# Kernel tuning notes

Measured on AMD Instinct MI355X. Metric: run time of the kernel, lower is better.

The kernel has to match this reference:

```python
import jax, jax.numpy as jnp
import numpy as np

EPS = 1e-6
BASE_THETA = 10000.0


def setup_inputs() -> dict:
    key = jax.random.key(0)
    ks = jax.random.split(key, 6)
    S, E = 4096, 4096
    scale = 1.0 / np.sqrt(E)
    return {
        "x": jax.random.normal(ks[0], (S, E), dtype=jnp.float32),
        "w_q": jax.random.normal(ks[1], (E, E), dtype=jnp.float32) * scale,
        "w_k": jax.random.normal(ks[2], (E, E), dtype=jnp.float32) * scale,
        "w_v": jax.random.normal(ks[3], (E, E), dtype=jnp.float32) * scale,
        "w_out": jax.random.normal(ks[4], (E, E), dtype=jnp.float32) * scale,
        "scaling_factor": jax.random.uniform(ks[5], (E,), dtype=jnp.float32, minval=0.5, maxval=1.5),
    }


def _rope_apply(t, cos, sin):
    # t: (S, D) fp16; cos/sin: (S, D//2) fp16. Closed form of the per-position
    # block-diagonal 2x2 rotation matrix matmul in the original loop:
    # out[2j]   =  t[2j]*cos + t[2j+1]*sin
    # out[2j+1] = -t[2j]*sin + t[2j+1]*cos
    S, D = t.shape
    t2 = t.reshape(S, D // 2, 2)
    even, odd = t2[..., 0], t2[..., 1]
    out = jnp.stack([even * cos + odd * sin, -even * sin + odd * cos], axis=-1)
    return out.reshape(S, D)


def reference(x, w_q, w_k, w_v, w_out, scaling_factor):
    f16, f32 = jnp.float16, jnp.float32
    S, E = x.shape
    # __init__: q / q_inv / head rotations are identity; quantize = cast fp16 (scale 1).
    # q_inv * scaling_factor.view(1,-1) == diag(scaling_factor) -> row-scale weights.
    wq = (scaling_factor[:, None] * w_q).astype(f16)
    wk = (scaling_factor[:, None] * w_k).astype(f16)
    wv = (scaling_factor[:, None] * w_v).astype(f16)
    wo = w_out.astype(f16)

    # input @ identity; rms_norm in fp32
    xn = x * jax.lax.rsqrt(jnp.mean(x * x, axis=-1, keepdims=True) + EPS)
    xq = xn.astype(f16)

    # quantized matmuls: fp16 operands, fp32 accumulation, cast back to fp16
    q = (xq.astype(f32) @ wq.astype(f32)).astype(f16)
    k = (xq.astype(f32) @ wk.astype(f32)).astype(f16)
    v = (xq.astype(f32) @ wv.astype(f32)).astype(f16)

    # RoPE over full feature dim (size = E), vectorized over positions
    pos = jnp.arange(S, dtype=f32)[:, None]
    j = jnp.arange(E // 2, dtype=f32)[None, :]
    theta = pos / jnp.power(BASE_THETA, 2.0 * j / E)
    cos = jnp.cos(theta).astype(f16)
    sin = jnp.sin(theta).astype(f16)
    q = _rope_apply(q, cos, sin)
    k = _rope_apply(k, cos, sin)

    # rot_head_k_tiled is identity -> quantize is just fp16 cast (already fp16)
    scores = (q.astype(f32) @ k.T.astype(f32)).astype(f16)
    scores = scores / np.float16(np.sqrt(E))
    # causal mask: strict upper triangle -> -inf
    row = jnp.arange(S)[:, None]
    col = jnp.arange(S)[None, :]
    scores = jnp.where(col > row, jnp.float16(-jnp.inf), scores)
    attn_w = jax.nn.softmax(scores, axis=1)
    attn = attn_w @ v  # fp16 matmul as in original

    out = (attn.astype(f32) @ wo.astype(f32)).astype(f16)
    return out
```

## Files before the change

kernel.cpp:

```cpp
#include <hip/hip_runtime.h>
#include <hip/hip_bf16.h>
#include <cmath>


typedef _Float16 f16;
typedef _Float16 f16x4 __attribute__((ext_vector_type(4)));
typedef _Float16 f16x8 __attribute__((ext_vector_type(8)));
typedef float f32x4 __attribute__((ext_vector_type(4)));

#define S_DIM 4096
#define E_DIM 4096

__device__ __forceinline__ void gload_lds16(const void* g, void* l) {
  __builtin_amdgcn_global_load_lds((const __attribute__((address_space(1))) void*)g,
                                   (__attribute__((address_space(3))) void*)l,
                                   16, 0, 0);
}

__global__ __launch_bounds__(256) void rmsnorm_f16(const float* __restrict__ x,
                                                   f16* __restrict__ xq, int E) {
  const int row = blockIdx.x;
  const int t = threadIdx.x;
  const float4* xr = (const float4*)(x + (size_t)row * E);
  float4 v[4];
  float ss = 0.f;
#pragma unroll
  for (int i = 0; i < 4; ++i) {
    v[i] = xr[t + 256 * i];
    ss += v[i].x * v[i].x + v[i].y * v[i].y + v[i].z * v[i].z + v[i].w * v[i].w;
  }
#pragma unroll
  for (int o = 1; o < 64; o <<= 1) ss += __shfl_xor(ss, o);
  __shared__ float red[4];
  const int wid = t >> 6, lane = t & 63;
  if (lane == 0) red[wid] = ss;
  __syncthreads();
  const float tot = red[0] + red[1] + red[2] + red[3];
  const float r = 1.0f / sqrtf(tot / (float)E + 1e-6f);
  f16* xo = xq + (size_t)row * E;
#pragma unroll
  for (int i = 0; i < 4; ++i) {
    f16x4 o;
    o[0] = (f16)(v[i].x * r);
    o[1] = (f16)(v[i].y * r);
    o[2] = (f16)(v[i].z * r);
    o[3] = (f16)(v[i].w * r);
    *(f16x4*)(xo + 4 * (t + 256 * i)) = o;
  }
}

__global__ __launch_bounds__(256) void wconv_t(const float* __restrict__ W,
                                               const float* __restrict__ s,
                                               f16* __restrict__ WT, int N) {
  __shared__ f16 tile[64][65];
  const int tr = blockIdx.y * 64;
  const int tc = blockIdx.x * 64;
  const int t = threadIdx.x;
  const int r = t / 16;
  const int c4 = (t % 16) * 4;
#pragma unroll
  for (int i = 0; i < 4; ++i) {
    const int row = r + i * 16;
    float4 w = *(const float4*)(W + (size_t)(tr + row) * N + tc + c4);
    const float sc = s ? s[tr + row] : 1.0f;
    tile[row][c4 + 0] = (f16)(w.x * sc);
    tile[row][c4 + 1] = (f16)(w.y * sc);
    tile[row][c4 + 2] = (f16)(w.z * sc);
    tile[row][c4 + 3] = (f16)(w.w * sc);
  }
  __syncthreads();
#pragma unroll
  for (int i = 0; i < 4; ++i) {
    const int row = r + i * 16;
    f16x4 o;
    o[0] = tile[c4 + 0][row];
    o[1] = tile[c4 + 1][row];
    o[2] = tile[c4 + 2][row];
    o[3] = tile[c4 + 3][row];
    *(f16x4*)(WT + (size_t)(tc + row) * N + tr + c4) = o;
  }
}

__global__ __launch_bounds__(256) void transpose_f16(const f16* __restrict__ V,
                                                     f16* __restrict__ VT,
                                                     int R, int C) {
  __shared__ f16 tile[64][65];
  const int tr = blockIdx.y * 64;
  const int tc = blockIdx.x * 64;
  const int t = threadIdx.x;
  const int r = t / 16;
  const int c4 = (t % 16) * 4;
#pragma unroll
  for (int i = 0; i < 4; ++i) {
    const int row = r + i * 16;
    f16x4 in = *(const f16x4*)(V + (size_t)(tr + row) * C + tc + c4);
    tile[row][c4 + 0] = in[0];
    tile[row][c4 + 1] = in[1];
    tile[row][c4 + 2] = in[2];
    tile[row][c4 + 3] = in[3];
  }
  __syncthreads();
#pragma unroll
  for (int i = 0; i < 4; ++i) {
    const int row = r + i * 16;
    f16x4 o;
    o[0] = tile[c4 + 0][row];
    o[1] = tile[c4 + 1][row];
    o[2] = tile[c4 + 2][row];
    o[3] = tile[c4 + 3][row];
    *(f16x4*)(VT + (size_t)(tc + row) * R + tr + c4) = o;
  }
}

__global__ __launch_bounds__(256) void freq_tab_k(float* __restrict__ tab) {
  const int j = blockIdx.x * 256 + threadIdx.x;
  if (j < 2048) tab[j] = (float)pow(10000.0, (double)j / 2048.0);
}

__global__ __launch_bounds__(256) void rope_qk(f16* __restrict__ q,
                                               f16* __restrict__ k,
                                               const float* __restrict__ ftab,
                                               int E) {
  const int idx = blockIdx.x * 256 + threadIdx.x;
  const int cpr = E / 8;
  const int pos = idx / cpr;
  const int ch = idx % cpr;
  const int j0 = ch * 4;
  const float fpos = (float)pos;
  f16x8 qv = *(f16x8*)(q + (size_t)idx * 8);
  f16x8 kv = *(f16x8*)(k + (size_t)idx * 8);
  f16x8 qo, ko;
#pragma unroll
  for (int p = 0; p < 4; ++p) {
    const int j = j0 + p;
    const float th = fpos / ftab[j];
    float sn, cs;
    sincosf(th, &sn, &cs);
    const f16 c16 = (f16)cs, s16 = (f16)sn;
    const float c = (float)c16, s = (float)s16;
    {
      const float e = (float)qv[2 * p], o = (float)qv[2 * p + 1];
      const f16 t1 = (f16)(e * c), t2 = (f16)(o * s);
      const f16 u1 = (f16)(-(e * s)), u2 = (f16)(o * c);
      qo[2 * p] = (f16)((float)t1 + (float)t2);
      qo[2 * p + 1] = (f16)((float)u1 + (float)u2);
    }
    {
      const float e = (float)kv[2 * p], o = (float)kv[2 * p + 1];
      const f16 t1 = (f16)(e * c), t2 = (f16)(o * s);
      const f16 u1 = (f16)(-(e * s)), u2 = (f16)(o * c);
      ko[2 * p] = (f16)((float)t1 + (float)t2);
      ko[2 * p + 1] = (f16)((float)u1 + (float)u2);
    }
  }
  *(f16x8*)(q + (size_t)idx * 8) = qo;
  *(f16x8*)(k + (size_t)idx * 8) = ko;
}

__global__ __launch_bounds__(256) void softmax_causal(f16* __restrict__ sc, int S) {
  const int row = blockIdx.x;
  const int t = threadIdx.x;
  f16* p = sc + (size_t)row * S;
  float v[16];
  bool msk[16];
#pragma unroll
  for (int i = 0; i < 2; ++i) {
    f16x8 a = *(const f16x8*)(p + (size_t)(i * 256 + t) * 8);
#pragma unroll
    for (int j = 0; j < 8; ++j) v[i * 8 + j] = (float)a[j];
  }
  float m = -1e30f;
#pragma unroll
  for (int i = 0; i < 2; ++i)
#pragma unroll
    for (int j = 0; j < 8; ++j) {
      const int col = (i * 256 + t) * 8 + j;
      const int ii = i * 8 + j;
      msk[ii] = (col > row);
      if (!msk[ii]) m = fmaxf(m, v[ii]);
    }
#pragma unroll
  for (int o = 1; o < 64; o <<= 1) m = fmaxf(m, __shfl_xor(m, o));
  __shared__ float red[4];
  const int wid = t >> 6, lane = t & 63;
  if (lane == 0) red[wid] = m;
  __syncthreads();
  m = fmaxf(fmaxf(red[0], red[1]), fmaxf(red[2], red[3]));
  __syncthreads();
  f16 e16[16];
  float sum = 0.f;
#pragma unroll
  for (int i = 0; i < 16; ++i) {
    if (msk[i]) {
      e16[i] = (f16)0.0f;
    } else {
      const f16 d16 = (f16)(v[i] - m);
      e16[i] = (f16)expf((float)d16);
      sum += (float)e16[i];
    }
  }
#pragma unroll
  for (int o = 1; o < 64; o <<= 1) sum += __shfl_xor(sum, o);
  if (lane == 0) red[wid] = sum;
  __syncthreads();
  sum = red[0] + red[1] + red[2] + red[3];
  const f16 den16 = (f16)sum;
  const float den = (float)den16;
#pragma unroll
  for (int i = 0; i < 2; ++i) {
    f16x8 o;
#pragma unroll
    for (int j = 0; j < 8; ++j) {
      const int ii = i * 8 + j;
      o[j] = msk[ii] ? (f16)0.0f : (f16)((float)e16[ii] / den);
    }
    *(f16x8*)(p + (size_t)(i * 256 + t) * 8) = o;
  }
}

__device__ __forceinline__ void store_out(f16* p, f16 v) { *p = v; }
__device__ __forceinline__ void store_out(float* p, f16 v) { *p = (float)v; }

template <typename OUT>
__global__ __launch_bounds__(512, 2) void gemm256(const f16* __restrict__ A,
                                                  const f16* __restrict__ BT,
                                                  OUT* __restrict__ C,
                                                  int M, int N, int K, float alpha,
                                                  int mode) {
  if (mode == 1 && blockIdx.x > blockIdx.y) return;
  const int bm = blockIdx.y * 256, bn = blockIdx.x * 256;
  const int kend = (mode == 2) ? (bm + 256 < K ? bm + 256 : K) : K;
  const int nt = kend >> 6;

  extern __shared__ char smem[];
  f16(*lds)[2][256][64] = (f16(*)[2][256][64])smem;

  const int tid = threadIdx.x;
  const int lane = tid & 63;
  const int wid = tid >> 6;
  const int wr = wid >> 2;
  const int wc = wid & 3;
  const f16* Ab = A + (size_t)bm * K;
  const f16* Bb = BT + (size_t)bn * K;

  const int l8 = lane >> 3;
  const int gxor8 = ((lane & 7) ^ l8) * 8;
  const int lr = lane & 15;
  const int shi = lane >> 4;
  const int rsw = lr & 7;

  auto STAGE = [&](int Ts, int hh) {
    const int k0 = Ts << 6;
    const int bsel = Ts & 1;
#pragma unroll
    for (int l = 0; l < 2; ++l) {
      const int rih0 = wid * 16 + l * 8;
      if (hh == 0 || hh == 3) {
        const int row0 = (rih0 & 63) + ((rih0 >> 6) << 7) + ((hh == 3) ? 64 : 0);
        gload_lds16(Ab + (size_t)(row0 + l8) * K + k0 + gxor8,
                    &lds[bsel][0][row0][0]);
      } else {
        const int row0 = (rih0 & 31) + ((rih0 >> 5) << 6) + ((hh == 2) ? 32 : 0);
        gload_lds16(Bb + (size_t)(row0 + l8) * K + k0 + gxor8,
                    &lds[bsel][1][row0][0]);
      }
    }
  };

  f32x4 acc[8][4] = {};

#pragma unroll
  for (int i = 0; i < 6; ++i) {
    const int Ts = i >> 2, hh = i & 3;
    if (Ts < nt) STAGE(Ts, hh);
  }

  for (int T = 0; T < nt; ++T) {
    const int cur = T & 1;
#pragma unroll
    for (int ph = 0; ph < 4; ++ph) {
      const int qm = ph >> 1, qn = ph & 1;
      asm volatile("s_waitcnt lgkmcnt(0)" ::: "memory");
      __builtin_amdgcn_sched_barrier(0);
      if (T + 1 < nt) {
        asm volatile("s_waitcnt vmcnt(8)" ::: "memory");
      } else {
        asm volatile("s_waitcnt vmcnt(0)" ::: "memory");
      }
      __builtin_amdgcn_sched_barrier(0);
      __builtin_amdgcn_s_barrier();
      __builtin_amdgcn_sched_barrier(0);
      {
        const int p6 = 4 * T + ph + 6;
        const int Ts = p6 >> 2, hh = p6 & 3;
        if (Ts < nt) STAGE(Ts, hh);
      }
      f16x8 af[4][2], bf[2][2];
#pragma unroll
      for (int m2 = 0; m2 < 4; ++m2)
#pragma unroll
        for (int kk = 0; kk < 2; ++kk)
          af[m2][kk] = *(const f16x8*)&lds[cur][0][wr * 128 + (qm * 4 + m2) * 16 + lr]
                                          [(((kk * 4 + shi) ^ rsw)) * 8];
#pragma unroll
      for (int n2 = 0; n2 < 2; ++n2)
#pragma unroll
        for (int kk = 0; kk < 2; ++kk)
          bf[n2][kk] = *(const f16x8*)&lds[cur][1][wc * 64 + (qn * 2 + n2) * 16 + lr]
                                          [(((kk * 4 + shi) ^ rsw)) * 8];
      __builtin_amdgcn_s_setprio(1);
#pragma unroll
      for (int m2 = 0; m2 < 4; ++m2)
#pragma unroll
        for (int n2 = 0; n2 < 2; ++n2)
#pragma unroll
          for (int kk = 0; kk < 2; ++kk)
            acc[qm * 4 + m2][qn * 2 + n2] = __builtin_amdgcn_mfma_f32_16x16x32_f16(
                af[m2][kk], bf[n2][kk], acc[qm * 4 + m2][qn * 2 + n2], 0, 0, 0);
      __builtin_amdgcn_s_setprio(0);
    }
  }

  const int rb = bm + wr * 128 + (lane >> 4) * 4;
  const int cb = bn + wc * 64 + (lane & 15);
#pragma unroll
  for (int mm = 0; mm < 8; ++mm)
#pragma unroll
    for (int nn = 0; nn < 4; ++nn) {
      const int col = cb + nn * 16;
#pragma unroll
      for (int r = 0; r < 4; ++r) {
        f16 h = (f16)acc[mm][nn][r];
        if (alpha != 1.0f) h = (f16)((float)h * alpha);
        store_out(&C[(size_t)(rb + mm * 16 + r) * N + col], h);
      }
    }
}

extern "C" void kernel_launch(void* const* d_in, const int* in_sizes, int n_in,
                              void* d_out, int out_size, void* d_ws, size_t ws_size,
                              hipStream_t stream) {
  const float* x = (const float*)d_in[0];
  const float* wq = (const float*)d_in[1];
  const float* wk = (const float*)d_in[2];
  const float* wv = (const float*)d_in[3];
  const float* wo = (const float*)d_in[4];
  const float* sf = (const float*)d_in[5];
  float* out = (float*)d_out;

  const int S = S_DIM, E = E_DIM;
  const size_t U = (size_t)S * E * sizeof(f16);
  char* ws = (char*)d_ws;
  f16* xq = (f16*)(ws + 0 * U);
  f16* wT = (f16*)(ws + 1 * U);
  f16* q  = (f16*)(ws + 2 * U);
  f16* k  = (f16*)(ws + 3 * U);
  f16* v  = (f16*)d_out;

  const int LDSB = 131072;
  hipFuncSetAttribute(reinterpret_cast<const void*>(&gemm256<f16>),
                      hipFuncAttributeMaxDynamicSharedMemorySize, LDSB);
  hipFuncSetAttribute(reinterpret_cast<const void*>(&gemm256<float>),
                      hipFuncAttributeMaxDynamicSharedMemorySize, LDSB);

  dim3 b256(256), b512(512);
  dim3 gT(E / 64, E / 64);
  dim3 gG(E / 256, S / 256);

  rmsnorm_f16<<<S, b256, 0, stream>>>(x, xq, E);

  wconv_t<<<gT, b256, 0, stream>>>(wq, sf, wT, E);
  gemm256<f16><<<gG, b512, LDSB, stream>>>(xq, wT, q, S, E, E, 1.0f, 0);
  wconv_t<<<gT, b256, 0, stream>>>(wk, sf, wT, E);
  gemm256<f16><<<gG, b512, LDSB, stream>>>(xq, wT, k, S, E, E, 1.0f, 0);
  wconv_t<<<gT, b256, 0, stream>>>(wv, sf, wT, E);
  gemm256<f16><<<gG, b512, LDSB, stream>>>(xq, wT, v, S, E, E, 1.0f, 0);

  float* ftab = (float*)wT;
  freq_tab_k<<<8, b256, 0, stream>>>(ftab);
  rope_qk<<<(S * (E / 8)) / 256, b256, 0, stream>>>(q, k, ftab, E);

  f16* sc = wT;
  gemm256<f16><<<dim3(S / 256, S / 256), b512, LDSB, stream>>>(q, k, sc, S, S, E,
                                                               1.0f / 64.0f, 1);
  softmax_causal<<<S, b256, 0, stream>>>(sc, S);

  f16* vT = xq;
  transpose_f16<<<dim3(E / 64, S / 64), b256, 0, stream>>>(v, vT, S, E);

  f16* attn = q;
  gemm256<f16><<<gG, b512, LDSB, stream>>>(sc, vT, attn, S, E, S, 1.0f, 2);

  f16* wT2 = k;
  wconv_t<<<gT, b256, 0, stream>>>(wo, (const float*)nullptr, wT2, E);
  gemm256<float><<<gG, b512, LDSB, stream>>>(attn, wT2, out, S, E, E, 1.0f, 0);
}
```

Measured before the change: 947.5 us.

## Restructure GEMM main loop into two half-phases with register-reused B fragments

Replaces the four quarter-phase LDS-read/MFMA steps per k-tile with two half-phases. B fragments for both column halves are loaded once into registers and reused across both A row halves, and A fragments are reloaded only once per half. Two staging loads are issued per barrier instead of one, which halves the number of barriers and waitcnt syncs per k-tile and cuts redundant LDS reads. The cost is higher register pressure from the extra held fragments, plus retuned vmcnt thresholds that must match the new load issue pattern.

```diff
diff --git a/kernel.cpp b/kernel.cpp
--- a/kernel.cpp
+++ b/kernel.cpp
@@ -249,7 +249,10 @@
   const int shi = lane >> 4;
   const int rsw = lr & 7;
 
-  auto STAGE = [&](int Ts, int hh) {
+  auto STAGE_P = [&](int p) {
+    const int c = p + 6;
+    const int Ts = c >> 2, hh = c & 3;
+    if (Ts >= nt) return;
     const int k0 = Ts << 6;
     const int bsel = Ts & 1;
 #pragma unroll
@@ -268,57 +271,94 @@
   };
 
   f32x4 acc[8][4] = {};
-
-#pragma unroll
-  for (int i = 0; i < 6; ++i) {
-    const int Ts = i >> 2, hh = i & 3;
-    if (Ts < nt) STAGE(Ts, hh);
-  }
+  f16x8 afr[4][2], b0r[2][2], b1r[2][2];
+
+#pragma unroll
+  for (int p = -6; p < 0; ++p) STAGE_P(p);
 
   for (int T = 0; T < nt; ++T) {
     const int cur = T & 1;
-#pragma unroll
-    for (int ph = 0; ph < 4; ++ph) {
-      const int qm = ph >> 1, qn = ph & 1;
-      asm volatile("s_waitcnt lgkmcnt(0)" ::: "memory");
-      __builtin_amdgcn_sched_barrier(0);
-      if (T + 1 < nt) {
-        asm volatile("s_waitcnt vmcnt(8)" ::: "memory");
-      } else {
-        asm volatile("s_waitcnt vmcnt(0)" ::: "memory");
+    asm volatile("s_waitcnt lgkmcnt(0)" ::: "memory");
+    __builtin_amdgcn_sched_barrier(0);
+    if (T + 1 < nt) {
+      asm volatile("s_waitcnt vmcnt(6)" ::: "memory");
+    } else {
+      asm volatile("s_waitcnt vmcnt(0)" ::: "memory");
+    }
+    __builtin_amdgcn_sched_barrier(0);
+    __builtin_amdgcn_s_barrier();
+    __builtin_amdgcn_sched_barrier(0);
+    STAGE_P(4 * T);
+    STAGE_P(4 * T + 1);
+#pragma unroll
+    for (int m2 = 0; m2 < 4; ++m2)
+#pragma unroll
+      for (int kk = 0; kk < 2; ++kk)
+        afr[m2][kk] = *(const f16x8*)&lds[cur][0][wr * 128 + m2 * 16 + lr]
+                                         [((kk * 4 + shi) ^ rsw) * 8];
+#pragma unroll
+    for (int n2 = 0; n2 < 2; ++n2)
+#pragma unroll
+      for (int kk = 0; kk < 2; ++kk) {
+        b0r[n2][kk] = *(const f16x8*)&lds[cur][1][wc * 64 + n2 * 16 + lr]
+                                         [((kk * 4 + shi) ^ rsw) * 8];
+        b1r[n2][kk] = *(const f16x8*)&lds[cur][1][wc * 64 + 32 + n2 * 16 + lr]
+                                         [((kk * 4 + shi) ^ rsw) * 8];
       }
-      __builtin_amdgcn_sched_barrier(0);
-      __builtin_amdgcn_s_barrier();
-      __builtin_amdgcn_sched_barrier(0);
-      {
-        const int p6 = 4 * T + ph + 6;
-        const int Ts = p6 >> 2, hh = p6 & 3;
-        if (Ts < nt) STAGE(Ts, hh);
-      }
-      f16x8 af[4][2], bf[2][2];
-#pragma unroll
-      for (int m2 = 0; m2 < 4; ++m2)
+    __builtin_amdgcn_s_setprio(1);
+#pragma unroll
+    for (int m2 = 0; m2 < 4; ++m2)
+#pragma unroll
+      for (int n2 = 0; n2 < 2; ++n2)
 #pragma unroll
         for (int kk = 0; kk < 2; ++kk)
-          af[m2][kk] = *(const f16x8*)&lds[cur][0][wr * 128 + (qm * 4 + m2) * 16 + lr]
-                                          [(((kk * 4 + shi) ^ rsw)) * 8];
+          acc[m2][n2] = __builtin_amdgcn_mfma_f32_16x16x32_f16(
+              afr[m2][kk], b0r[n2][kk], acc[m2][n2], 0, 0, 0);
+#pragma unroll
+    for (int m2 = 0; m2 < 4; ++m2)
 #pragma unroll
       for (int n2 = 0; n2 < 2; ++n2)
 #pragma unroll
         for (int kk = 0; kk < 2; ++kk)
-          bf[n2][kk] = *(const f16x8*)&lds[cur][1][wc * 64 + (qn * 2 + n2) * 16 + lr]
-                                          [(((kk * 4 + shi) ^ rsw)) * 8];
-      __builtin_amdgcn_s_setprio(1);
-#pragma unroll
-      for (int m2 = 0; m2 < 4; ++m2)
-#pragma unroll
-        for (int n2 = 0; n2 < 2; ++n2)
-#pragma unroll
-          for (int kk = 0; kk < 2; ++kk)
-            acc[qm * 4 + m2][qn * 2 + n2] = __builtin_amdgcn_mfma_f32_16x16x32_f16(
-                af[m2][kk], bf[n2][kk], acc[qm * 4 + m2][qn * 2 + n2], 0, 0, 0);
-      __builtin_amdgcn_s_setprio(0);
-    }
+          acc[m2][2 + n2] = __builtin_amdgcn_mfma_f32_16x16x32_f16(
+              afr[m2][kk], b1r[n2][kk], acc[m2][2 + n2], 0, 0, 0);
+    __builtin_amdgcn_s_setprio(0);
+    asm volatile("s_waitcnt lgkmcnt(0)" ::: "memory");
+    __builtin_amdgcn_sched_barrier(0);
+    if (T + 1 < nt) {
+      asm volatile("s_waitcnt vmcnt(8)" ::: "memory");
+    } else {
+      asm volatile("s_waitcnt vmcnt(0)" ::: "memory");
+    }
+    __builtin_amdgcn_sched_barrier(0);
+    __builtin_amdgcn_s_barrier();
+    __builtin_amdgcn_sched_barrier(0);
+    STAGE_P(4 * T + 2);
+    STAGE_P(4 * T + 3);
+#pragma unroll
+    for (int m2 = 0; m2 < 4; ++m2)
+#pragma unroll
+      for (int kk = 0; kk < 2; ++kk)
+        afr[m2][kk] = *(const f16x8*)&lds[cur][0][wr * 128 + 64 + m2 * 16 + lr]
+                                         [((kk * 4 + shi) ^ rsw) * 8];
+    __builtin_amdgcn_s_setprio(1);
+#pragma unroll
+    for (int m2 = 0; m2 < 4; ++m2)
+#pragma unroll
+      for (int n2 = 0; n2 < 2; ++n2)
+#pragma unroll
+        for (int kk = 0; kk < 2; ++kk)
+          acc[4 + m2][2 + n2] = __builtin_amdgcn_mfma_f32_16x16x32_f16(
+              afr[m2][kk], b1r[n2][kk], acc[4 + m2][2 + n2], 0, 0, 0);
+#pragma unroll
+    for (int m2 = 0; m2 < 4; ++m2)
+#pragma unroll
+      for (int n2 = 0; n2 < 2; ++n2)
+#pragma unroll
+        for (int kk = 0; kk < 2; ++kk)
+          acc[4 + m2][n2] = __builtin_amdgcn_mfma_f32_16x16x32_f16(
+              afr[m2][kk], b0r[n2][kk], acc[4 + m2][n2], 0, 0, 0);
+    __builtin_amdgcn_s_setprio(0);
   }
 
   const int rb = bm + wr * 128 + (lane >> 4) * 4;
```

Measured after the change: 833.6 us. 12.0% less time.
